# Optimization experiments

Hardware: AMD Instinct MI355X
Metric: run time of the kernel (lower is better)

Reference implementation:

```python
import jax, jax.numpy as jnp
import numpy as np

HEAD_SIZE = 64
INPUT_SIZE = 1024
B, T = 8, 2048


def setup_inputs() -> dict:
    key = jax.random.key(0)
    kx, kq, kk, kv = jax.random.split(key, 4)
    x = jax.random.normal(kx, (B, T, INPUT_SIZE), dtype=jnp.float32)
    s = 1.0 / np.sqrt(INPUT_SIZE)
    Wq = jax.random.uniform(kq, (INPUT_SIZE, HEAD_SIZE), minval=-s, maxval=s, dtype=jnp.float32)
    Wk = jax.random.uniform(kk, (INPUT_SIZE, HEAD_SIZE), minval=-s, maxval=s, dtype=jnp.float32)
    Wv = jax.random.uniform(kv, (INPUT_SIZE, HEAD_SIZE), minval=-s, maxval=s, dtype=jnp.float32)
    return {"x": x, "Wq": Wq, "Wk": Wk, "Wv": Wv}


def reference(x, Wq, Wk, Wv):
    # Faithful to the torch module: scores = K @ Q^T (note: keys times queries^T),
    # causal mask on upper triangle of that matrix, softmax over last axis,
    # dropout treated as identity (eval), then scores @ V.
    q = jnp.einsum('bti,ih->bth', x, Wq)  # [B,T,H]
    k = jnp.einsum('bti,ih->bth', x, Wk)
    v = jnp.einsum('bti,ih->bth', x, Wv)
    scale = HEAD_SIZE ** -0.5
    scores = jnp.einsum('bth,bsh->bts', k, q) * scale  # [B,T,T] = K Q^T
    Tlen = x.shape[1]
    causal = jnp.tril(jnp.ones((Tlen, Tlen), dtype=bool))
    scores = jnp.where(causal, scores, -jnp.inf)
    w = jax.nn.softmax(scores, axis=-1)
    out = jnp.einsum('bts,bsh->bth', w, v)  # [B,T,H]
    return out
```

## Files before the change

kernel.cpp:

```cpp
#include <hip/hip_runtime.h>

typedef __bf16 bf16_t;
typedef bf16_t bf16x8 __attribute__((ext_vector_type(8)));
typedef float f32x4 __attribute__((ext_vector_type(4)));

#define NB 8
#define TT 2048
#define DIN 1024
#define HH 64
#define MM (NB * TT)

__device__ __forceinline__ unsigned short f2bf(float f) {
    unsigned int u = __float_as_uint(f);
    u += 0x7fffu + ((u >> 16) & 1u);
    return (unsigned short)(u >> 16);
}

__device__ __forceinline__ void async16(void* l, const void* g) {
    __builtin_amdgcn_global_load_lds(
        (const __attribute__((address_space(1))) unsigned int*)g,
        (__attribute__((address_space(3))) unsigned int*)l, 16, 0, 0);
}

__device__ __forceinline__ int block_detect_f32(const unsigned int* __restrict__ xw,
                                                int tid, int* sflag) {
    if (tid < 64) {
        unsigned int u = xw[tid];
        unsigned int e = (u >> 7) & 0xFFu;
        unsigned long long m = __ballot(e >= 100u && e <= 150u);
        if (tid == 0) *sflag = (__popcll(m) < 48) ? 1 : 0;
    }
    __syncthreads();
    return *sflag;
}

__global__ __launch_bounds__(256) void transpose_w_kernel(
    const void* __restrict__ Wq, const void* __restrict__ Wk,
    const void* __restrict__ Wv, const unsigned int* __restrict__ xw,
    unsigned short* __restrict__ Wt) {
    __shared__ int sflag;
    __shared__ unsigned short ts[64][68];
    const int tid = threadIdx.x;
    const int isf32 = block_detect_f32(xw, tid, &sflag);
    const int w = blockIdx.x >> 4, kt = blockIdx.x & 15;
    const void* W = (w == 0) ? Wq : (w == 1) ? Wk : Wv;
    const int kk = tid >> 4, nn = (tid & 15) * 4;
#pragma unroll
    for (int j = 0; j < 4; ++j) {
        int k = kk + j * 16;
        if (isf32) {
            float4 f = *(const float4*)((const float*)W + (size_t)(kt * 64 + k) * 64 + nn);
            ts[k][nn + 0] = f2bf(f.x); ts[k][nn + 1] = f2bf(f.y);
            ts[k][nn + 2] = f2bf(f.z); ts[k][nn + 3] = f2bf(f.w);
        } else {
            *(uint2*)&ts[k][nn] =
                *(const uint2*)((const unsigned short*)W + (size_t)(kt * 64 + k) * 64 + nn);
        }
    }
    __syncthreads();
    const int n = tid >> 2, k0 = (tid & 3) * 16;
    unsigned short tmp[16];
#pragma unroll
    for (int j = 0; j < 16; ++j) tmp[j] = ts[k0 + j][n];
    unsigned short* dst = Wt + (size_t)(w * 64 + n) * 1024 + kt * 64 + k0;
    *(uint4*)(dst + 0) = *(uint4*)&tmp[0];
    *(uint4*)(dst + 8) = *(uint4*)&tmp[8];
}

#define XR 72
#define WROWC 9

__global__ __launch_bounds__(256, 2) void proj_kernel(
    const void* __restrict__ xraw, const unsigned short* __restrict__ Wt,
    unsigned short* __restrict__ qbuf, unsigned short* __restrict__ kbuf,
    unsigned short* __restrict__ vtbuf) {
    __shared__ int sflag;
    __shared__ __align__(16) unsigned short xs[64 * XR];
    __shared__ __align__(16) unsigned char wlds[96 * WROWC * 16];

    const int tid = threadIdx.x;
    const int isf32 = block_detect_f32((const unsigned int*)xraw, tid, &sflag);
    const int m0 = blockIdx.x * 64;
    const int nh = blockIdx.y;
    const int wave = tid >> 6, lane = tid & 63, quad = lane >> 4, l15 = lane & 15;
    const int rw = wave & 1, cw = wave >> 1;

    const float* xf = (const float*)xraw;
    const unsigned short* xb = (const unsigned short*)xraw;
    const unsigned char* wg = (const unsigned char*)Wt;

    const unsigned char* wsrc[4];
    unsigned int wdst[4];
    int nw = 0;
#pragma unroll
    for (int j = 0; j < 4; ++j) {
        int c = (wave + 4 * j) * 64 + lane;
        if (c < 864) {
            int R = c / WROWC, cc = c % WROWC;
            int ccu = (cc > 7) ? 0 : cc;
            wsrc[nw] = wg + (size_t)(nh * 96 + R) * 2048 + ccu * 16;
            wdst[nw] = c * 16;
            ++nw;
        }
    }

    const int xr = tid >> 2, xc = (tid & 3) * 16;
    float4 px[4];
    uint4  pxb[2];
    auto ldx = [&](int k0) {
        if (isf32) {
            const float* g = xf + (size_t)(m0 + xr) * DIN + k0 + xc;
#pragma unroll
            for (int j = 0; j < 4; ++j) px[j] = *(const float4*)(g + j * 4);
        } else {
            const unsigned short* g = xb + (size_t)(m0 + xr) * DIN + k0 + xc;
            pxb[0] = *(const uint4*)(g + 0);
            pxb[1] = *(const uint4*)(g + 8);
        }
    };

    f32x4 acc[2][3];
#pragma unroll
    for (int rt = 0; rt < 2; ++rt)
#pragma unroll
        for (int ct = 0; ct < 3; ++ct)
            acc[rt][ct] = (f32x4){0.f, 0.f, 0.f, 0.f};

    ldx(0);
    size_t woff = 0;
    for (int it = 0; it < 16; ++it) {
        __syncthreads();
        if (isf32) {
            unsigned short t[16];
#pragma unroll
            for (int j = 0; j < 4; ++j) {
                t[j * 4 + 0] = f2bf(px[j].x); t[j * 4 + 1] = f2bf(px[j].y);
                t[j * 4 + 2] = f2bf(px[j].z); t[j * 4 + 3] = f2bf(px[j].w);
            }
            *(uint4*)&xs[xr * XR + xc + 0] = *(uint4*)&t[0];
            *(uint4*)&xs[xr * XR + xc + 8] = *(uint4*)&t[8];
        } else {
            *(uint4*)&xs[xr * XR + xc + 0] = pxb[0];
            *(uint4*)&xs[xr * XR + xc + 8] = pxb[1];
        }
        for (int j = 0; j < nw; ++j) async16(&wlds[wdst[j]], wsrc[j] + woff);
        woff += 128;
        __syncthreads();

        if (it < 15) ldx((it + 1) * 64);

#pragma unroll
        for (int ks = 0; ks < 2; ++ks) {
            bf16x8 a[2], b[3];
#pragma unroll
            for (int rt = 0; rt < 2; ++rt)
                a[rt] = *(const bf16x8*)
                    &xs[(rw * 32 + rt * 16 + l15) * XR + ks * 32 + quad * 8];
#pragma unroll
            for (int ct = 0; ct < 3; ++ct)
                b[ct] = *(const bf16x8*)
                    &wlds[(cw * 48 + ct * 16 + l15) * (WROWC * 16) + ks * 64 + quad * 16];
#pragma unroll
            for (int rt = 0; rt < 2; ++rt)
#pragma unroll
                for (int ct = 0; ct < 3; ++ct)
                    acc[rt][ct] = __builtin_amdgcn_mfma_f32_16x16x32_bf16(
                        a[rt], b[ct], acc[rt][ct], 0, 0, 0);
        }
    }

#pragma unroll
    for (int rt = 0; rt < 2; ++rt)
#pragma unroll
        for (int ct = 0; ct < 3; ++ct) {
            int n = nh * 96 + cw * 48 + ct * 16 + l15;
            int wsel = n >> 6, nn = n & 63;
#pragma unroll
            for (int reg = 0; reg < 4; ++reg) {
                int m = m0 + rw * 32 + rt * 16 + quad * 4 + reg;
                unsigned short bv = f2bf(acc[rt][ct][reg]);
                if (wsel == 0)      qbuf[(size_t)m * HH + nn] = bv;
                else if (wsel == 1) kbuf[(size_t)m * HH + nn] = bv;
                else {
                    int bb = m >> 11, t = m & 2047;
                    vtbuf[((size_t)bb * HH + nn) * TT + t] = bv;
                }
            }
        }
}

__global__ __launch_bounds__(256) void attn_kernel(
    const unsigned short* __restrict__ rowbuf,
    const unsigned short* __restrict__ colbuf,
    const unsigned short* __restrict__ vtbuf,
    float* __restrict__ O_part,
    float* __restrict__ l_part) {

    __shared__ __align__(16) unsigned short Qr_s[64][72];
    __shared__ __align__(16) unsigned short Kc_s[64][72];
    __shared__ __align__(16) unsigned short Vt_s[64][72];
    __shared__ __align__(16) unsigned short P_s[4][16][72];

    const int tid  = threadIdx.x;
    const int bx   = blockIdx.x;
    const int b    = blockIdx.y;
    int rt, ch;
    if (bx < 8)       { rt = bx;                 ch = 0; }
    else if (bx < 24) { rt = 8 + ((bx - 8) >> 1);  ch = (bx - 8) & 1; }
    else if (bx < 48) { rt = 16 + (bx - 24) / 3;   ch = (bx - 24) % 3; }
    else              { rt = 24 + ((bx - 48) >> 2); ch = (bx - 48) & 3; }
    const int nct = min(8, rt + 1 - ch * 8);
    const int t0 = rt * 64;
    const int slot = b * 80 + bx;

    const int wave = tid >> 6, lane = tid & 63, quad = lane >> 4, l15 = lane & 15;
    const int sr = tid >> 2, sc = (tid & 3) * 16;

    {
        const uint4* g = (const uint4*)(rowbuf + ((size_t)b * TT + t0 + sr) * HH + sc);
        *(uint4*)&Qr_s[sr][sc + 0] = g[0];
        *(uint4*)&Qr_s[sr][sc + 8] = g[1];
    }

    f32x4 o[4];
#pragma unroll
    for (int c = 0; c < 4; ++c) o[c] = (f32x4){0.f, 0.f, 0.f, 0.f};
    float ls[4] = {0.f, 0.f, 0.f, 0.f};

    const float SCL2 = 0.125f * 1.4426950408889634f;

    for (int i = 0; i < nct; ++i) {
        const int stc = ch * 8 + i;
        const int s0 = stc * 64;
        {
            const uint4* gk = (const uint4*)(colbuf + ((size_t)b * TT + s0 + sr) * HH + sc);
            uint4 k0 = gk[0], k1 = gk[1];
            const uint4* gv = (const uint4*)(vtbuf + ((size_t)b * HH + sr) * TT + s0 + sc);
            uint4 v0 = gv[0], v1 = gv[1];
            *(uint4*)&Kc_s[sr][sc + 0] = k0;
            *(uint4*)&Kc_s[sr][sc + 8] = k1;
            *(uint4*)&Vt_s[sr][sc + 0] = v0;
            *(uint4*)&Vt_s[sr][sc + 8] = v1;
        }
        __syncthreads();

        f32x4 scf[4];
#pragma unroll
        for (int c = 0; c < 4; ++c) scf[c] = (f32x4){0.f, 0.f, 0.f, 0.f};
#pragma unroll
        for (int ks = 0; ks < 2; ++ks) {
            bf16x8 a = *(const bf16x8*)&Qr_s[wave * 16 + l15][ks * 32 + quad * 8];
#pragma unroll
            for (int c = 0; c < 4; ++c) {
                bf16x8 bb = *(const bf16x8*)&Kc_s[c * 16 + l15][ks * 32 + quad * 8];
                scf[c] = __builtin_amdgcn_mfma_f32_16x16x32_bf16(a, bb, scf[c], 0, 0, 0);
            }
        }

        const bool diag = (stc == rt);
#pragma unroll
        for (int r = 0; r < 4; ++r) {
            const int tg = t0 + wave * 16 + quad * 4 + r;
#pragma unroll
            for (int c = 0; c < 4; ++c) {
                float arg = fmaf(scf[c][r], SCL2, -30.f);
                if (diag && (s0 + c * 16 + l15) > tg) arg = -200.f;
                float p = __builtin_amdgcn_exp2f(arg);
                P_s[wave][quad * 4 + r][c * 16 + l15] = f2bf(p);
                ls[r] += p;
            }
        }
#pragma unroll
        for (int ks = 0; ks < 2; ++ks) {
            bf16x8 ap = *(const bf16x8*)&P_s[wave][l15][ks * 32 + quad * 8];
#pragma unroll
            for (int c = 0; c < 4; ++c) {
                bf16x8 bv = *(const bf16x8*)&Vt_s[c * 16 + l15][ks * 32 + quad * 8];
                o[c] = __builtin_amdgcn_mfma_f32_16x16x32_bf16(ap, bv, o[c], 0, 0, 0);
            }
        }
        __syncthreads();
    }

#pragma unroll
    for (int r = 0; r < 4; ++r) {
#pragma unroll
        for (int off = 1; off < 16; off <<= 1) ls[r] += __shfl_xor(ls[r], off);
    }
    if (l15 == 0) {
#pragma unroll
        for (int r = 0; r < 4; ++r)
            l_part[(size_t)slot * 64 + wave * 16 + quad * 4 + r] = ls[r];
    }
#pragma unroll
    for (int c = 0; c < 4; ++c)
#pragma unroll
        for (int r = 0; r < 4; ++r)
            O_part[(size_t)slot * 4096 + (wave * 16 + quad * 4 + r) * 64 + c * 16 + l15] = o[c][r];
}

__global__ __launch_bounds__(256) void combine_kernel(
    const float* __restrict__ O_part, const float* __restrict__ l_part,
    const unsigned int* __restrict__ xw, void* __restrict__ outraw) {
    __shared__ int sflag;
    const int tid = threadIdx.x;
    const int isf32 = block_detect_f32(xw, tid, &sflag);
    const int rt = blockIdx.x, b = blockIdx.y;
    const int nch = rt / 8 + 1;
    const int off = (rt < 8) ? rt : (rt < 16) ? 8 + 2 * (rt - 8)
                   : (rt < 24) ? 24 + 3 * (rt - 16) : 48 + 4 * (rt - 24);
    const int slot0 = b * 80 + off;

    const int row = tid >> 2, cb = (tid & 3) * 16;
    f32x4 a[4];
#pragma unroll
    for (int q = 0; q < 4; ++q) a[q] = (f32x4){0.f, 0.f, 0.f, 0.f};
    float l = 0.f;
    for (int j = 0; j < nch; ++j) {
        const f32x4* p = (const f32x4*)(O_part + (size_t)(slot0 + j) * 4096 + row * 64 + cb);
#pragma unroll
        for (int q = 0; q < 4; ++q) a[q] += p[q];
        l += l_part[(size_t)(slot0 + j) * 64 + row];
    }
    const float inv = 1.f / l;
    const size_t base = ((size_t)b * TT + rt * 64 + row) * HH + cb;
    if (isf32) {
        float* outf = (float*)outraw;
#pragma unroll
        for (int q = 0; q < 4; ++q) {
            f32x4 v = a[q] * inv;
            *(f32x4*)(outf + base + q * 4) = v;
        }
    } else {
        unsigned short h[16];
#pragma unroll
        for (int q = 0; q < 4; ++q)
#pragma unroll
            for (int e = 0; e < 4; ++e) h[q * 4 + e] = f2bf(a[q][e] * inv);
        unsigned short* outb = (unsigned short*)outraw;
        *(uint4*)(outb + base + 0) = *(uint4*)&h[0];
        *(uint4*)(outb + base + 8) = *(uint4*)&h[8];
    }
}

extern "C" void kernel_launch(void* const* d_in, const int* in_sizes, int n_in,
                              void* d_out, int out_size, void* d_ws, size_t ws_size,
                              hipStream_t stream) {
    const void* x  = d_in[0];
    const void* Wq = d_in[1];
    const void* Wk = d_in[2];
    const void* Wv = d_in[3];
    unsigned short* ws = (unsigned short*)d_ws;

    unsigned short* qbuf  = ws;
    unsigned short* kbuf  = ws + (size_t)MM * HH;
    unsigned short* vtbuf = ws + (size_t)2 * MM * HH;
    unsigned short* wtbuf = ws + (size_t)3 * MM * HH;
    float* O_part = (float*)(ws + (size_t)3 * MM * HH + 3 * 65536);
    float* l_part = O_part + (size_t)640 * 4096;

    hipLaunchKernelGGL(transpose_w_kernel, dim3(48), dim3(256), 0, stream,
                       Wq, Wk, Wv, (const unsigned int*)x, wtbuf);
    hipLaunchKernelGGL(proj_kernel, dim3(256, 2), dim3(256), 0, stream,
                       x, wtbuf, qbuf, kbuf, vtbuf);
    hipLaunchKernelGGL(attn_kernel, dim3(80, 8), dim3(256), 0, stream,
                       kbuf, qbuf, vtbuf, O_part, l_part);
    hipLaunchKernelGGL(combine_kernel, dim3(32, 8), dim3(256), 0, stream,
                       O_part, l_part, (const unsigned int*)x, d_out);
}
```

Before: 144.8 us.

## Double-buffer projection LDS, prefetch K/V in attention, swizzle block mapping

The projection kernel now uses double-buffered LDS for the x and W tiles. The next tile is staged while the current one is computed, which removes one barrier per iteration. The attention kernel prefetches the next K/V tile into registers during the softmax and PV stage. All three kernels use 1D grids with swizzled block-to-work mapping to improve L2 locality and spread batches across CUs, and attention gets a launch-bounds occupancy hint. The cost is double the LDS in projection and more register pressure.

```diff
diff --git a/kernel.cpp b/kernel.cpp
--- a/kernel.cpp
+++ b/kernel.cpp
@@ -75,13 +75,15 @@
     unsigned short* __restrict__ qbuf, unsigned short* __restrict__ kbuf,
     unsigned short* __restrict__ vtbuf) {
     __shared__ int sflag;
-    __shared__ __align__(16) unsigned short xs[64 * XR];
-    __shared__ __align__(16) unsigned char wlds[96 * WROWC * 16];
+    __shared__ __align__(16) unsigned short xs[2][64 * XR];
+    __shared__ __align__(16) unsigned char wlds[2][96 * WROWC * 16];
 
     const int tid = threadIdx.x;
     const int isf32 = block_detect_f32((const unsigned int*)xraw, tid, &sflag);
-    const int m0 = blockIdx.x * 64;
-    const int nh = blockIdx.y;
+    const int bid = blockIdx.x;
+    const int swz = (bid & 7) * 64 + (bid >> 3);
+    const int nh = swz & 1;
+    const int m0 = (swz >> 1) * 64;
     const int wave = tid >> 6, lane = tid & 63, quad = lane >> 4, l15 = lane & 15;
     const int rw = wave & 1, cw = wave >> 1;
 
@@ -118,18 +120,7 @@
             pxb[1] = *(const uint4*)(g + 8);
         }
     };
-
-    f32x4 acc[2][3];
-#pragma unroll
-    for (int rt = 0; rt < 2; ++rt)
-#pragma unroll
-        for (int ct = 0; ct < 3; ++ct)
-            acc[rt][ct] = (f32x4){0.f, 0.f, 0.f, 0.f};
-
-    ldx(0);
-    size_t woff = 0;
-    for (int it = 0; it < 16; ++it) {
-        __syncthreads();
+    auto writeX = [&](int buf) {
         if (isf32) {
             unsigned short t[16];
 #pragma unroll
@@ -137,29 +128,37 @@
                 t[j * 4 + 0] = f2bf(px[j].x); t[j * 4 + 1] = f2bf(px[j].y);
                 t[j * 4 + 2] = f2bf(px[j].z); t[j * 4 + 3] = f2bf(px[j].w);
             }
-            *(uint4*)&xs[xr * XR + xc + 0] = *(uint4*)&t[0];
-            *(uint4*)&xs[xr * XR + xc + 8] = *(uint4*)&t[8];
+            *(uint4*)&xs[buf][xr * XR + xc + 0] = *(uint4*)&t[0];
+            *(uint4*)&xs[buf][xr * XR + xc + 8] = *(uint4*)&t[8];
         } else {
-            *(uint4*)&xs[xr * XR + xc + 0] = pxb[0];
-            *(uint4*)&xs[xr * XR + xc + 8] = pxb[1];
-        }
-        for (int j = 0; j < nw; ++j) async16(&wlds[wdst[j]], wsrc[j] + woff);
-        woff += 128;
-        __syncthreads();
-
-        if (it < 15) ldx((it + 1) * 64);
-
+            *(uint4*)&xs[buf][xr * XR + xc + 0] = pxb[0];
+            *(uint4*)&xs[buf][xr * XR + xc + 8] = pxb[1];
+        }
+    };
+    auto stageW = [&](int buf, int itk) {
+        const size_t off = (size_t)itk * 128;
+        for (int j = 0; j < nw; ++j) async16(&wlds[buf][wdst[j]], wsrc[j] + off);
+    };
+
+    f32x4 acc[2][3];
+#pragma unroll
+    for (int rt = 0; rt < 2; ++rt)
+#pragma unroll
+        for (int ct = 0; ct < 3; ++ct)
+            acc[rt][ct] = (f32x4){0.f, 0.f, 0.f, 0.f};
+
+    auto compute = [&](int buf) {
 #pragma unroll
         for (int ks = 0; ks < 2; ++ks) {
             bf16x8 a[2], b[3];
 #pragma unroll
             for (int rt = 0; rt < 2; ++rt)
                 a[rt] = *(const bf16x8*)
-                    &xs[(rw * 32 + rt * 16 + l15) * XR + ks * 32 + quad * 8];
+                    &xs[buf][(rw * 32 + rt * 16 + l15) * XR + ks * 32 + quad * 8];
 #pragma unroll
             for (int ct = 0; ct < 3; ++ct)
                 b[ct] = *(const bf16x8*)
-                    &wlds[(cw * 48 + ct * 16 + l15) * (WROWC * 16) + ks * 64 + quad * 16];
+                    &wlds[buf][(cw * 48 + ct * 16 + l15) * (WROWC * 16) + ks * 64 + quad * 16];
 #pragma unroll
             for (int rt = 0; rt < 2; ++rt)
 #pragma unroll
@@ -167,6 +166,22 @@
                     acc[rt][ct] = __builtin_amdgcn_mfma_f32_16x16x32_bf16(
                         a[rt], b[ct], acc[rt][ct], 0, 0, 0);
         }
+    };
+
+    ldx(0);
+    writeX(0);
+    stageW(0, 0);
+    ldx(64);
+    __syncthreads();
+
+    for (int it = 0; it < 16; ++it) {
+        if (it < 15) {
+            writeX((it + 1) & 1);
+            stageW((it + 1) & 1, it + 1);
+            if (it < 14) ldx((it + 2) * 64);
+        }
+        compute(it & 1);
+        __syncthreads();
     }
 
 #pragma unroll
@@ -189,7 +204,7 @@
         }
 }
 
-__global__ __launch_bounds__(256) void attn_kernel(
+__global__ __launch_bounds__(256, 4) void attn_kernel(
     const unsigned short* __restrict__ rowbuf,
     const unsigned short* __restrict__ colbuf,
     const unsigned short* __restrict__ vtbuf,
@@ -202,8 +217,9 @@
     __shared__ __align__(16) unsigned short P_s[4][16][72];
 
     const int tid  = threadIdx.x;
-    const int bx   = blockIdx.x;
-    const int b    = blockIdx.y;
+    const int bid  = blockIdx.x;
+    const int b    = bid & 7;
+    const int bx   = bid >> 3;
     int rt, ch;
     if (bx < 8)       { rt = bx;                 ch = 0; }
     else if (bx < 24) { rt = 8 + ((bx - 8) >> 1);  ch = (bx - 8) & 1; }
@@ -229,19 +245,23 @@
 
     const float SCL2 = 0.125f * 1.4426950408889634f;
 
+    uint4 pk0, pk1, pv0, pv1;
+    auto loadKV = [&](int i) {
+        const int s0 = (ch * 8 + i) * 64;
+        const uint4* gk = (const uint4*)(colbuf + ((size_t)b * TT + s0 + sr) * HH + sc);
+        pk0 = gk[0]; pk1 = gk[1];
+        const uint4* gv = (const uint4*)(vtbuf + ((size_t)b * HH + sr) * TT + s0 + sc);
+        pv0 = gv[0]; pv1 = gv[1];
+    };
+    loadKV(0);
+
     for (int i = 0; i < nct; ++i) {
         const int stc = ch * 8 + i;
         const int s0 = stc * 64;
-        {
-            const uint4* gk = (const uint4*)(colbuf + ((size_t)b * TT + s0 + sr) * HH + sc);
-            uint4 k0 = gk[0], k1 = gk[1];
-            const uint4* gv = (const uint4*)(vtbuf + ((size_t)b * HH + sr) * TT + s0 + sc);
-            uint4 v0 = gv[0], v1 = gv[1];
-            *(uint4*)&Kc_s[sr][sc + 0] = k0;
-            *(uint4*)&Kc_s[sr][sc + 8] = k1;
-            *(uint4*)&Vt_s[sr][sc + 0] = v0;
-            *(uint4*)&Vt_s[sr][sc + 8] = v1;
-        }
+        *(uint4*)&Kc_s[sr][sc + 0] = pk0;
+        *(uint4*)&Kc_s[sr][sc + 8] = pk1;
+        *(uint4*)&Vt_s[sr][sc + 0] = pv0;
+        *(uint4*)&Vt_s[sr][sc + 8] = pv1;
         __syncthreads();
 
         f32x4 scf[4];
@@ -256,6 +276,8 @@
                 scf[c] = __builtin_amdgcn_mfma_f32_16x16x32_bf16(a, bb, scf[c], 0, 0, 0);
             }
         }
+
+        if (i + 1 < nct) loadKV(i + 1);
 
         const bool diag = (stc == rt);
 #pragma unroll
@@ -305,7 +327,8 @@
     __shared__ int sflag;
     const int tid = threadIdx.x;
     const int isf32 = block_detect_f32(xw, tid, &sflag);
-    const int rt = blockIdx.x, b = blockIdx.y;
+    const int bid = blockIdx.x;
+    const int b = bid & 7, rt = bid >> 3;
     const int nch = rt / 8 + 1;
     const int off = (rt < 8) ? rt : (rt < 16) ? 8 + 2 * (rt - 8)
                    : (rt < 24) ? 24 + 3 * (rt - 16) : 48 + 4 * (rt - 24);
@@ -361,10 +384,10 @@
 
     hipLaunchKernelGGL(transpose_w_kernel, dim3(48), dim3(256), 0, stream,
                        Wq, Wk, Wv, (const unsigned int*)x, wtbuf);
-    hipLaunchKernelGGL(proj_kernel, dim3(256, 2), dim3(256), 0, stream,
+    hipLaunchKernelGGL(proj_kernel, dim3(512), dim3(256), 0, stream,
                        x, wtbuf, qbuf, kbuf, vtbuf);
-    hipLaunchKernelGGL(attn_kernel, dim3(80, 8), dim3(256), 0, stream,
+    hipLaunchKernelGGL(attn_kernel, dim3(640), dim3(256), 0, stream,
                        kbuf, qbuf, vtbuf, O_part, l_part);
-    hipLaunchKernelGGL(combine_kernel, dim3(32, 8), dim3(256), 0, stream,
+    hipLaunchKernelGGL(combine_kernel, dim3(256), dim3(256), 0, stream,
                        O_part, l_part, (const unsigned int*)x, d_out);
 }
```

New measurement: 175.4 us. 1.21x slower.
